# Kernel optimization log

Measured on AMD Instinct MI355X. Metric: run time of the kernel, lower is better.

Reference implementation:

```python
import jax, jax.numpy as jnp
import numpy as np

ALPHA = 0.2  # LeakyReLU negative slope
B, N, F, T, H, D = 4, 2048, 256, 8, 4, 64


def setup_inputs() -> dict:
    key = jax.random.key(0)
    ks = jax.random.split(key, 8)
    x = jax.random.normal(ks[0], (B, N, F), dtype=jnp.float32)
    adj = jax.random.randint(ks[1], (B, N, N), 0, 2, dtype=jnp.int32)
    type_idx = jax.random.randint(ks[2], (B, N), 0, T)
    type_onehot = jax.nn.one_hot(type_idx, T, dtype=jnp.float32)
    # per-head parameters stacked on a leading head axis (original uses H separate layers)
    s = 0.06  # ~xavier_uniform scale for these fan sizes
    Wq = jax.random.normal(ks[3], (H, F + T, D), dtype=jnp.float32) * s
    Wk = jax.random.normal(ks[4], (H, F + T, D), dtype=jnp.float32) * s
    W = jax.random.normal(ks[5], (H, F, D), dtype=jnp.float32) * s
    a = jax.random.normal(ks[6], (H, 2 * D, 1), dtype=jnp.float32) * s
    return {"x": x, "adj": adj, "type_onehot": type_onehot,
            "Wq": Wq, "Wk": Wk, "W": W, "a": a}


def reference(x, adj, type_onehot, Wq, Wk, W, a):
    # eval mode: dropout is identity
    nh, d = W.shape[0], W.shape[2]
    h_t = jnp.concatenate([x, type_onehot], axis=-1)           # (B,N,F+T)
    q = jnp.einsum('bnf,hfd->bhnd', h_t, Wq)                   # (B,H,N,D)
    k = jnp.einsum('bnf,hfd->bhnd', h_t, Wk)                   # (B,H,N,D)
    a1 = a[:, :d, 0]                                           # (H,D)
    a2 = a[:, d:, 0]                                           # (H,D)
    e1 = jnp.einsum('bhnd,hd->bhn', q, a1)                     # (B,H,N)
    e2 = jnp.einsum('bhnd,hd->bhn', k, a2)                     # (B,H,N)
    e = e1[:, :, :, None] + e2[:, :, None, :]                  # (B,H,N,N) additive score
    e = jnp.where(e > 0, e, ALPHA * e)                         # leaky relu
    mask = (adj > 0)[:, None, :, :]                            # (B,1,N,N)
    att = jnp.where(mask, e, jnp.float32(-9e15))
    att = jax.nn.softmax(att, axis=2)                          # torch dim=1 of (B,N,N) == axis 2 here
    att = att * adj[:, None, :, :].astype(att.dtype)
    Wh = jnp.einsum('bnf,hfd->bhnd', x, W)                     # (B,H,N,D)
    h_prime = jnp.einsum('bhij,bhjd->bhid', att, Wh)           # (B,H,N,D)
    out = jax.nn.elu(h_prime)                                  # concat=True per head
    # concat heads on feature dim, matching torch.cat([...], dim=2)
    return out.transpose(0, 2, 1, 3).reshape(x.shape[0], x.shape[1], nh * d)
```

## Files before the change

### kernel.cpp

```cpp
#include <hip/hip_runtime.h>
#include <hip/hip_bf16.h>
#include <math.h>

#define ALPHA 0.2f
#define LOG2E 1.4426950408889634f

constexpr int B_ = 4, N_ = 2048, F_ = 256, T_ = 8, H_ = 4, D_ = 64;
constexpr int FT = F_ + T_;

using half8   = __attribute__((ext_vector_type(8))) _Float16;
using float4v = __attribute__((ext_vector_type(4))) float;
using uint4v  = __attribute__((ext_vector_type(4))) unsigned;

#if __has_builtin(__builtin_amdgcn_exp2f)
#define EXP2F(x) __builtin_amdgcn_exp2f(x)
#else
#define EXP2F(x) exp2f(x)
#endif

__device__ inline unsigned pkrtz_u(float a, float b) {
    return __builtin_bit_cast(unsigned, __builtin_amdgcn_cvt_pkrtz(a, b));
}

#define V1_OFF    0u
#define V2_OFF    4224u
#define E1A_OFF   8448u
#define E2A_OFF   270592u
#define PARTS_OFF 794880u
#define WT_OFF    2892032u
#define BITS_OFF  3023104u
#define WHT_OFF   5120256u

__device__ inline void gl2lds16(const void* g, void* l) {
    __builtin_amdgcn_global_load_lds(
        (const __attribute__((address_space(1))) unsigned*)g,
        (__attribute__((address_space(3))) unsigned*)l, 16, 0, 0);
}

__global__ __launch_bounds__(256) void k_pre(const int* __restrict__ adj,
                                             const float* __restrict__ Wq,
                                             const float* __restrict__ Wk,
                                             const float* __restrict__ a,
                                             const float* __restrict__ W,
                                             unsigned* __restrict__ bits,
                                             float* __restrict__ v1,
                                             float* __restrict__ v2,
                                             _Float16* __restrict__ WT) {
    if (blockIdx.x < 65536u) {
        size_t tid = (size_t)blockIdx.x * 256 + threadIdx.x;
        int av = adj[tid];
        unsigned long long msk = __ballot(av != 0);
        int lane = threadIdx.x & 63;
        if (lane == 0)       bits[tid >> 5] = (unsigned)msk;
        else if (lane == 32) bits[tid >> 5] = (unsigned)(msk >> 32);
        return;
    }
    int gid = (blockIdx.x - 65536) * 256 + threadIdx.x;
    if (gid < 65536) {
        int hd = gid >> 8, f = gid & 255;
        int h = hd >> 6, d = hd & 63;
        WT[(size_t)hd * F_ + f] = (_Float16)W[((size_t)h * F_ + f) * D_ + d];
        return;
    }
    int tid = gid - 65536;
    if (tid >= 2 * H_ * FT) return;
    int sel = tid / (H_ * FT);
    int r = tid - sel * (H_ * FT);
    int h = r / FT, f = r - h * FT;
    const float* Wx = sel ? Wk : Wq;
    const float* av = a + h * 2 * D_ + sel * D_;
    const float* wrow = Wx + (size_t)(h * FT + f) * D_;
    float acc = 0.f;
    for (int d = 0; d < D_; ++d) acc += wrow[d] * av[d];
    (sel ? v2 : v1)[h * FT + f] = acc * LOG2E;
}

__global__ __launch_bounds__(256) void k_mid(const float* __restrict__ x,
                                             const float* __restrict__ oh,
                                             const float* __restrict__ v1,
                                             const float* __restrict__ v2,
                                             const _Float16* __restrict__ WT,
                                             float2* __restrict__ E1A,
                                             float2* __restrict__ E2A,
                                             _Float16* __restrict__ WhT) {
    if (blockIdx.x < 2048u) {
        int lane = threadIdx.x & 63;
        int w = threadIdx.x >> 6;
        int bn = blockIdx.x * 4 + w;
        int b = bn >> 11, n = bn & (N_ - 1);
        float a1h[H_] = {0.f, 0.f, 0.f, 0.f};
        float a2h[H_] = {0.f, 0.f, 0.f, 0.f};
        const float* xrow = x + (size_t)(b * N_ + n) * F_;
        for (int c = 0; c < 4; ++c) {
            int f = c * 64 + lane;
            float xv = xrow[f];
            #pragma unroll
            for (int h = 0; h < H_; ++h) {
                a1h[h] += xv * v1[h * FT + f];
                a2h[h] += xv * v2[h * FT + f];
            }
        }
        if (lane < T_) {
            float ov = oh[(size_t)(b * N_ + n) * T_ + lane];
            #pragma unroll
            for (int h = 0; h < H_; ++h) {
                a1h[h] += ov * v1[h * FT + F_ + lane];
                a2h[h] += ov * v2[h * FT + F_ + lane];
            }
        }
        #pragma unroll
        for (int off = 32; off; off >>= 1) {
            #pragma unroll
            for (int h = 0; h < H_; ++h) {
                a1h[h] += __shfl_xor(a1h[h], off, 64);
                a2h[h] += __shfl_xor(a2h[h], off, 64);
            }
        }
        if (lane == 0) {
            #pragma unroll
            for (int h = 0; h < H_; ++h) {
                size_t o = (size_t)(b * H_ + h) * N_ + n;
                E1A[o] = {EXP2F(a1h[h]), EXP2F(ALPHA * a1h[h])};
                E2A[o] = {EXP2F(a2h[h]), EXP2F(ALPHA * a2h[h])};
            }
        }
        return;
    }
    int bid = blockIdx.x - 2048;
    int jt = bid & 127, b = bid >> 7;
    int lane = threadIdx.x & 63;
    int h = threadIdx.x >> 6;
    int j0 = jt * 16;
    int m = lane & 15, quad = lane >> 4;
    float4v zero = {0.f, 0.f, 0.f, 0.f};
    float4v acc[4] = {zero, zero, zero, zero};
    #pragma unroll 2
    for (int f0 = 0; f0 < F_; f0 += 32) {
        const float* xp = x + (size_t)(b * N_ + j0 + m) * F_ + f0 + quad * 8;
        float4v xlo = *(const float4v*)xp;
        float4v xhi = *(const float4v*)(xp + 4);
        uint4v bp = {pkrtz_u(xlo[0], xlo[1]), pkrtz_u(xlo[2], xlo[3]),
                     pkrtz_u(xhi[0], xhi[1]), pkrtz_u(xhi[2], xhi[3])};
        half8 bfrag = __builtin_bit_cast(half8, bp);
        #pragma unroll
        for (int mt = 0; mt < 4; ++mt) {
            const _Float16* ap = WT + (size_t)(h * 64 + mt * 16 + m) * F_ + f0 + quad * 8;
            half8 afrag = *(const half8*)ap;
            acc[mt] = __builtin_amdgcn_mfma_f32_16x16x32_f16(afrag, bfrag, acc[mt], 0, 0, 0);
        }
    }
    #pragma unroll
    for (int mt = 0; mt < 4; ++mt) {
        #pragma unroll
        for (int reg = 0; reg < 4; ++reg) {
            int hd = h * 64 + mt * 16 + quad * 4 + reg;
            WhT[((size_t)b * 256 + hd) * N_ + j0 + m] = (_Float16)acc[mt][reg];
        }
    }
}

__global__ __launch_bounds__(256) void k_colsum(const unsigned* __restrict__ bits,
                                                const float2* __restrict__ E1A,
                                                const float2* __restrict__ E2A,
                                                float* __restrict__ part_s) {
    int tid = threadIdx.x;
    int jt = blockIdx.x, b = blockIdx.y, ic = blockIdx.z;
    int j = jt * 256 + tid;
    int i0 = ic * 128;
    float2 e2v[H_];
    float acc[H_] = {0.f, 0.f, 0.f, 0.f};
    #pragma unroll
    for (int h = 0; h < H_; ++h) e2v[h] = E2A[(size_t)(b * H_ + h) * N_ + j];
    const float2* e1b = E1A + (size_t)(b * H_) * N_;
    const unsigned* bp = bits + ((size_t)(b * N_ + i0)) * 64 + (j >> 5);
    unsigned sh = j & 31;
    #pragma unroll 8
    for (int k = 0; k < 128; ++k) {
        unsigned wv = bp[(size_t)k * 64];
        bool on = (wv >> sh) & 1u;
        int i = i0 + k;
        #pragma unroll
        for (int h = 0; h < H_; ++h) {
            float2 e1 = e1b[h * N_ + i];
            float t = fmaxf(e1.x * e2v[h].x, e1.y * e2v[h].y);
            acc[h] += on ? t : 0.f;
        }
    }
    #pragma unroll
    for (int h = 0; h < H_; ++h)
        part_s[(size_t)ic * (B_ * H_ * N_) + (size_t)(b * H_ + h) * N_ + j] = acc[h];
}

__global__ __launch_bounds__(256, 2) void k_main(const unsigned* __restrict__ bits,
                                                 const float2* __restrict__ E1A,
                                                 const float2* __restrict__ E2A,
                                                 const float* __restrict__ parts,
                                                 const _Float16* __restrict__ WhT,
                                                 float* __restrict__ out) {
    __shared__ float sPC[2048];
    __shared__ float sNC[2048];
    __shared__ unsigned sLUT[256][4];
    __shared__ _Float16 sW[2][8192];
    int lane = threadIdx.x;
    int wy = threadIdx.y;
    int it = blockIdx.x;
    int b  = blockIdx.y;
    int h  = blockIdx.z;
    int ibase = it * 64 + wy * 16;
    int m = lane & 15, quad = lane >> 4;
    int bh = b * H_ + h;
    int t256 = wy * 64 + lane;

    {
        unsigned t = t256;
        sLUT[t][0] = ((t & 1u) ? 0xFFFFu : 0u) | ((t & 2u) ? 0xFFFF0000u : 0u);
        sLUT[t][1] = ((t & 4u) ? 0xFFFFu : 0u) | ((t & 8u) ? 0xFFFF0000u : 0u);
        sLUT[t][2] = ((t & 16u) ? 0xFFFFu : 0u) | ((t & 32u) ? 0xFFFF0000u : 0u);
        sLUT[t][3] = ((t & 64u) ? 0xFFFFu : 0u) | ((t & 128u) ? 0xFFFF0000u : 0u);
        int base = t256 * 8;
        float4v s0 = {0.f, 0.f, 0.f, 0.f}, s1 = {0.f, 0.f, 0.f, 0.f};
        #pragma unroll
        for (int ic = 0; ic < 16; ++ic) {
            const float* pp = parts + (size_t)ic * (B_ * H_ * N_) + (size_t)bh * N_ + base;
            s0 += *(const float4v*)pp;
            s1 += *(const float4v*)(pp + 4);
        }
        const float2* e2p = E2A + (size_t)bh * N_ + base;
        #pragma unroll
        for (int e = 0; e < 4; ++e) {
            float s = s0[e];
            float c = (s > 0.f) ? 1.f / s : 0.f;
            float2 e2 = e2p[e];
            sPC[base + e] = e2.x * c;
            sNC[base + e] = e2.y * c;
        }
        #pragma unroll
        for (int e = 0; e < 4; ++e) {
            float s = s1[e];
            float c = (s > 0.f) ? 1.f / s : 0.f;
            float2 e2 = e2p[4 + e];
            sPC[base + 4 + e] = e2.x * c;
            sNC[base + 4 + e] = e2.y * c;
        }
    }
    float2 e1v = E1A[(size_t)bh * N_ + ibase + m];
    const _Float16* bbase = WhT + (size_t)(b * 256 + h * 64) * N_;
    const unsigned* brow = bits + ((size_t)(b * N_) + ibase + m) * 64;

    auto stage = [&](int buf, int jb) {
        #pragma unroll
        for (int q = 0; q < 4; ++q) {
            int r = q * 16 + wy * 4 + (lane >> 4);
            int g = (lane & 15) ^ (r & 15);
            const _Float16* gp = bbase + (size_t)r * N_ + jb + g * 8;
            void* lp = (void*)&sW[buf][q * 2048 + wy * 512];
            gl2lds16(gp, lp);
        }
    };

    stage(0, 0);
    __syncthreads();

    float4v zero = {0.f, 0.f, 0.f, 0.f};
    float4v acc[4] = {zero, zero, zero, zero};

    for (int k = 0; k < 16; ++k) {
        if (k < 15) stage((k + 1) & 1, (k + 1) * 128);
        uint4v bwv = *(const uint4v*)(brow + k * 4);
        #pragma unroll
        for (int u = 0; u < 4; ++u) {
            unsigned byte = (bwv[u] >> (quad * 8)) & 0xFFu;
            uint4v msk = *(const uint4v*)&sLUT[byte][0];
            int jg = k * 128 + u * 32 + quad * 8;
            float4v p0 = *(const float4v*)&sPC[jg];
            float4v p1 = *(const float4v*)&sPC[jg + 4];
            float4v n0 = *(const float4v*)&sNC[jg];
            float4v n1 = *(const float4v*)&sNC[jg + 4];
            float w[8];
            #pragma unroll
            for (int e = 0; e < 4; ++e) w[e]     = fmaxf(e1v.x * p0[e], e1v.y * n0[e]);
            #pragma unroll
            for (int e = 0; e < 4; ++e) w[4 + e] = fmaxf(e1v.x * p1[e], e1v.y * n1[e]);
            uint4v wvp = {pkrtz_u(w[0], w[1]) & msk[0], pkrtz_u(w[2], w[3]) & msk[1],
                          pkrtz_u(w[4], w[5]) & msk[2], pkrtz_u(w[6], w[7]) & msk[3]};
            half8 afrag = __builtin_bit_cast(half8, wvp);
            #pragma unroll
            for (int dt = 0; dt < 4; ++dt) {
                int r = dt * 16 + m;
                int segp = (u * 4 + quad) ^ m;
                half8 bfrag = *(const half8*)&sW[k & 1][r * 128 + segp * 8];
                acc[dt] = __builtin_amdgcn_mfma_f32_16x16x32_f16(afrag, bfrag, acc[dt], 0, 0, 0);
            }
        }
        __syncthreads();
    }

    #pragma unroll
    for (int dt = 0; dt < 4; ++dt) {
        #pragma unroll
        for (int reg = 0; reg < 4; ++reg) {
            int i = ibase + quad * 4 + reg;
            int d = dt * 16 + m;
            float v = acc[dt][reg];
            v = v > 0.f ? v : expm1f(v);
            out[((size_t)(b * N_ + i)) * (H_ * D_) + h * D_ + d] = v;
        }
    }
}

extern "C" void kernel_launch(void* const* d_in, const int* in_sizes, int n_in,
                              void* d_out, int out_size, void* d_ws, size_t ws_size,
                              hipStream_t stream) {
    const float* x   = (const float*)d_in[0];
    const int*   adj = (const int*)d_in[1];
    const float* oh  = (const float*)d_in[2];
    const float* Wq  = (const float*)d_in[3];
    const float* Wk  = (const float*)d_in[4];
    const float* W   = (const float*)d_in[5];
    const float* a   = (const float*)d_in[6];
    float* out = (float*)d_out;
    char* ws = (char*)d_ws;

    float*   v1    = (float*)(ws + V1_OFF);
    float*   v2    = (float*)(ws + V2_OFF);
    float2*  E1A   = (float2*)(ws + E1A_OFF);
    float2*  E2A   = (float2*)(ws + E2A_OFF);
    float*   parts = (float*)(ws + PARTS_OFF);
    _Float16* WT   = (_Float16*)(ws + WT_OFF);
    unsigned* bits = (unsigned*)(ws + BITS_OFF);
    _Float16* WhT  = (_Float16*)(ws + WHT_OFF);

    k_pre<<<65536 + 265, 256, 0, stream>>>(adj, Wq, Wk, a, W, bits, v1, v2, WT);
    k_mid<<<2048 + 512, 256, 0, stream>>>(x, oh, v1, v2, WT, E1A, E2A, WhT);
    k_colsum<<<dim3(8, 4, 16), 256, 0, stream>>>(bits, E1A, E2A, parts);
    k_main<<<dim3(32, 4, 4), dim3(64, 4), 0, stream>>>(bits, E1A, E2A, parts, WhT, out);
}
```

Baseline: 187.4 us.

## Vectorize adjacency bit-packing, cache E1 in LDS, double rows per wave in main

Adjacency packing now has each thread read four ints as a vector and combine nibbles with xor-shuffles, so the kernel needs a quarter as many blocks. The column-sum kernel stages E1 values in shared memory instead of rereading them from global memory every iteration. The main kernel gives each wave two 16-row tiles that share the staged WhT B-fragments and the sPC/sNC loads, which halves its grid. The LDS lookup table for masking is replaced by per-element selects. The cost is more registers per thread and fewer blocks in the main kernel, which may lower occupancy and parallelism.

```diff
diff --git a/kernel.cpp b/kernel.cpp
--- a/kernel.cpp
+++ b/kernel.cpp
@@ -10,6 +10,7 @@
 
 using half8   = __attribute__((ext_vector_type(8))) _Float16;
 using float4v = __attribute__((ext_vector_type(4))) float;
+using int4v   = __attribute__((ext_vector_type(4))) int;
 using uint4v  = __attribute__((ext_vector_type(4))) unsigned;
 
 #if __has_builtin(__builtin_amdgcn_exp2f)
@@ -46,16 +47,20 @@
                                              float* __restrict__ v1,
                                              float* __restrict__ v2,
                                              _Float16* __restrict__ WT) {
-    if (blockIdx.x < 65536u) {
-        size_t tid = (size_t)blockIdx.x * 256 + threadIdx.x;
-        int av = adj[tid];
-        unsigned long long msk = __ballot(av != 0);
+    if (blockIdx.x < 16384u) {
+        size_t t = (size_t)blockIdx.x * 256 + threadIdx.x;
         int lane = threadIdx.x & 63;
-        if (lane == 0)       bits[tid >> 5] = (unsigned)msk;
-        else if (lane == 32) bits[tid >> 5] = (unsigned)(msk >> 32);
+        int4v av = ((const int4v*)adj)[t];
+        unsigned nib = (av.x != 0 ? 1u : 0u) | (av.y != 0 ? 2u : 0u) |
+                       (av.z != 0 ? 4u : 0u) | (av.w != 0 ? 8u : 0u);
+        unsigned v = nib << ((lane & 7) * 4);
+        v |= __shfl_xor(v, 1, 64);
+        v |= __shfl_xor(v, 2, 64);
+        v |= __shfl_xor(v, 4, 64);
+        if ((lane & 7) == 0) bits[t >> 3] = v;
         return;
     }
-    int gid = (blockIdx.x - 65536) * 256 + threadIdx.x;
+    int gid = (blockIdx.x - 16384) * 256 + threadIdx.x;
     if (gid < 65536) {
         int hd = gid >> 8, f = gid & 255;
         int h = hd >> 6, d = hd & 63;
@@ -163,25 +168,31 @@
                                                 const float2* __restrict__ E1A,
                                                 const float2* __restrict__ E2A,
                                                 float* __restrict__ part_s) {
+    __shared__ float2 sE1[H_][128];
     int tid = threadIdx.x;
     int jt = blockIdx.x, b = blockIdx.y, ic = blockIdx.z;
     int j = jt * 256 + tid;
     int i0 = ic * 128;
+    #pragma unroll
+    for (int r = 0; r < 2; ++r) {
+        int idx = r * 256 + tid;
+        int hh = idx >> 7, ii = idx & 127;
+        sE1[hh][ii] = E1A[(size_t)(b * H_ + hh) * N_ + i0 + ii];
+    }
     float2 e2v[H_];
     float acc[H_] = {0.f, 0.f, 0.f, 0.f};
     #pragma unroll
     for (int h = 0; h < H_; ++h) e2v[h] = E2A[(size_t)(b * H_ + h) * N_ + j];
-    const float2* e1b = E1A + (size_t)(b * H_) * N_;
+    __syncthreads();
     const unsigned* bp = bits + ((size_t)(b * N_ + i0)) * 64 + (j >> 5);
     unsigned sh = j & 31;
     #pragma unroll 8
     for (int k = 0; k < 128; ++k) {
         unsigned wv = bp[(size_t)k * 64];
         bool on = (wv >> sh) & 1u;
-        int i = i0 + k;
         #pragma unroll
         for (int h = 0; h < H_; ++h) {
-            float2 e1 = e1b[h * N_ + i];
+            float2 e1 = sE1[h][k];
             float t = fmaxf(e1.x * e2v[h].x, e1.y * e2v[h].y);
             acc[h] += on ? t : 0.f;
         }
@@ -199,24 +210,18 @@
                                                  float* __restrict__ out) {
     __shared__ float sPC[2048];
     __shared__ float sNC[2048];
-    __shared__ unsigned sLUT[256][4];
     __shared__ _Float16 sW[2][8192];
     int lane = threadIdx.x;
     int wy = threadIdx.y;
     int it = blockIdx.x;
     int b  = blockIdx.y;
     int h  = blockIdx.z;
-    int ibase = it * 64 + wy * 16;
+    int ibase = it * 128 + wy * 32;
     int m = lane & 15, quad = lane >> 4;
     int bh = b * H_ + h;
     int t256 = wy * 64 + lane;
 
     {
-        unsigned t = t256;
-        sLUT[t][0] = ((t & 1u) ? 0xFFFFu : 0u) | ((t & 2u) ? 0xFFFF0000u : 0u);
-        sLUT[t][1] = ((t & 4u) ? 0xFFFFu : 0u) | ((t & 8u) ? 0xFFFF0000u : 0u);
-        sLUT[t][2] = ((t & 16u) ? 0xFFFFu : 0u) | ((t & 32u) ? 0xFFFF0000u : 0u);
-        sLUT[t][3] = ((t & 64u) ? 0xFFFFu : 0u) | ((t & 128u) ? 0xFFFF0000u : 0u);
         int base = t256 * 8;
         float4v s0 = {0.f, 0.f, 0.f, 0.f}, s1 = {0.f, 0.f, 0.f, 0.f};
         #pragma unroll
@@ -243,9 +248,11 @@
             sNC[base + 4 + e] = e2.y * c;
         }
     }
-    float2 e1v = E1A[(size_t)bh * N_ + ibase + m];
+    float2 e1vA = E1A[(size_t)bh * N_ + ibase + m];
+    float2 e1vB = E1A[(size_t)bh * N_ + ibase + 16 + m];
     const _Float16* bbase = WhT + (size_t)(b * 256 + h * 64) * N_;
-    const unsigned* brow = bits + ((size_t)(b * N_) + ibase + m) * 64;
+    const unsigned* browA = bits + ((size_t)(b * N_) + ibase + m) * 64;
+    const unsigned* browB = bits + ((size_t)(b * N_) + ibase + 16 + m) * 64;
 
     auto stage = [&](int buf, int jb) {
         #pragma unroll
@@ -262,34 +269,47 @@
     __syncthreads();
 
     float4v zero = {0.f, 0.f, 0.f, 0.f};
-    float4v acc[4] = {zero, zero, zero, zero};
+    float4v accA[4] = {zero, zero, zero, zero};
+    float4v accB[4] = {zero, zero, zero, zero};
 
     for (int k = 0; k < 16; ++k) {
         if (k < 15) stage((k + 1) & 1, (k + 1) * 128);
-        uint4v bwv = *(const uint4v*)(brow + k * 4);
+        uint4v bwA = *(const uint4v*)(browA + k * 4);
+        uint4v bwB = *(const uint4v*)(browB + k * 4);
         #pragma unroll
         for (int u = 0; u < 4; ++u) {
-            unsigned byte = (bwv[u] >> (quad * 8)) & 0xFFu;
-            uint4v msk = *(const uint4v*)&sLUT[byte][0];
+            unsigned wqA = bwA[u] >> (quad * 8);
+            unsigned wqB = bwB[u] >> (quad * 8);
             int jg = k * 128 + u * 32 + quad * 8;
             float4v p0 = *(const float4v*)&sPC[jg];
             float4v p1 = *(const float4v*)&sPC[jg + 4];
             float4v n0 = *(const float4v*)&sNC[jg];
             float4v n1 = *(const float4v*)&sNC[jg + 4];
-            float w[8];
-            #pragma unroll
-            for (int e = 0; e < 4; ++e) w[e]     = fmaxf(e1v.x * p0[e], e1v.y * n0[e]);
-            #pragma unroll
-            for (int e = 0; e < 4; ++e) w[4 + e] = fmaxf(e1v.x * p1[e], e1v.y * n1[e]);
-            uint4v wvp = {pkrtz_u(w[0], w[1]) & msk[0], pkrtz_u(w[2], w[3]) & msk[1],
-                          pkrtz_u(w[4], w[5]) & msk[2], pkrtz_u(w[6], w[7]) & msk[3]};
-            half8 afrag = __builtin_bit_cast(half8, wvp);
+            float wA[8], wB[8];
+            #pragma unroll
+            for (int e = 0; e < 4; ++e) {
+                float tA0 = fmaxf(e1vA.x * p0[e], e1vA.y * n0[e]);
+                float tA1 = fmaxf(e1vA.x * p1[e], e1vA.y * n1[e]);
+                wA[e]     = (wqA & (1u << e))  ? tA0 : 0.f;
+                wA[4 + e] = (wqA & (16u << e)) ? tA1 : 0.f;
+                float tB0 = fmaxf(e1vB.x * p0[e], e1vB.y * n0[e]);
+                float tB1 = fmaxf(e1vB.x * p1[e], e1vB.y * n1[e]);
+                wB[e]     = (wqB & (1u << e))  ? tB0 : 0.f;
+                wB[4 + e] = (wqB & (16u << e)) ? tB1 : 0.f;
+            }
+            uint4v wpA = {pkrtz_u(wA[0], wA[1]), pkrtz_u(wA[2], wA[3]),
+                          pkrtz_u(wA[4], wA[5]), pkrtz_u(wA[6], wA[7])};
+            uint4v wpB = {pkrtz_u(wB[0], wB[1]), pkrtz_u(wB[2], wB[3]),
+                          pkrtz_u(wB[4], wB[5]), pkrtz_u(wB[6], wB[7])};
+            half8 afA = __builtin_bit_cast(half8, wpA);
+            half8 afB = __builtin_bit_cast(half8, wpB);
             #pragma unroll
             for (int dt = 0; dt < 4; ++dt) {
                 int r = dt * 16 + m;
                 int segp = (u * 4 + quad) ^ m;
                 half8 bfrag = *(const half8*)&sW[k & 1][r * 128 + segp * 8];
-                acc[dt] = __builtin_amdgcn_mfma_f32_16x16x32_f16(afrag, bfrag, acc[dt], 0, 0, 0);
+                accA[dt] = __builtin_amdgcn_mfma_f32_16x16x32_f16(afA, bfrag, accA[dt], 0, 0, 0);
+                accB[dt] = __builtin_amdgcn_mfma_f32_16x16x32_f16(afB, bfrag, accB[dt], 0, 0, 0);
             }
         }
         __syncthreads();
@@ -299,11 +319,14 @@
     for (int dt = 0; dt < 4; ++dt) {
         #pragma unroll
         for (int reg = 0; reg < 4; ++reg) {
-            int i = ibase + quad * 4 + reg;
+            int iA = ibase + quad * 4 + reg;
             int d = dt * 16 + m;
-            float v = acc[dt][reg];
-            v = v > 0.f ? v : expm1f(v);
-            out[((size_t)(b * N_ + i)) * (H_ * D_) + h * D_ + d] = v;
+            float vA = accA[dt][reg];
+            vA = vA > 0.f ? vA : expm1f(vA);
+            out[((size_t)(b * N_ + iA)) * (H_ * D_) + h * D_ + d] = vA;
+            float vB = accB[dt][reg];
+            vB = vB > 0.f ? vB : expm1f(vB);
+            out[((size_t)(b * N_ + iA + 16)) * (H_ * D_) + h * D_ + d] = vB;
         }
     }
 }
@@ -330,8 +353,8 @@
     unsigned* bits = (unsigned*)(ws + BITS_OFF);
     _Float16* WhT  = (_Float16*)(ws + WHT_OFF);
 
-    k_pre<<<65536 + 265, 256, 0, stream>>>(adj, Wq, Wk, a, W, bits, v1, v2, WT);
+    k_pre<<<16384 + 265, 256, 0, stream>>>(adj, Wq, Wk, a, W, bits, v1, v2, WT);
     k_mid<<<2048 + 512, 256, 0, stream>>>(x, oh, v1, v2, WT, E1A, E2A, WhT);
     k_colsum<<<dim3(8, 4, 16), 256, 0, stream>>>(bits, E1A, E2A, parts);
-    k_main<<<dim3(32, 4, 4), dim3(64, 4), 0, stream>>>(bits, E1A, E2A, parts, WhT, out);
-}
+    k_main<<<dim3(16, 4, 4), dim3(64, 4), 0, stream>>>(bits, E1A, E2A, parts, WhT, out);
+}
```

New measurement: 180.4 us. 1.04x faster.

## Vectorize adjacency bit-packing, stage E1 in LDS, replace mask LUT with selects

Applied to the files above, without the earlier changes.

The adjacency packing kernel now has each thread load four ints as one vector and builds each 32-bit mask word with shuffle-xor reductions. This cuts the grid to a quarter of its size and widens the global loads on a bandwidth-bound pass. The column-sum kernel preloads its E1 slice into shared memory instead of rereading it from global for every row. The main kernel drops the 256-entry LDS mask lookup table and applies bits with per-element selects, trading LDS traffic for extra VALU work.

```diff
diff --git a/kernel.cpp b/kernel.cpp
--- a/kernel.cpp
+++ b/kernel.cpp
@@ -10,6 +10,7 @@
 
 using half8   = __attribute__((ext_vector_type(8))) _Float16;
 using float4v = __attribute__((ext_vector_type(4))) float;
+using int4v   = __attribute__((ext_vector_type(4))) int;
 using uint4v  = __attribute__((ext_vector_type(4))) unsigned;
 
 #if __has_builtin(__builtin_amdgcn_exp2f)
@@ -46,16 +47,20 @@
                                              float* __restrict__ v1,
                                              float* __restrict__ v2,
                                              _Float16* __restrict__ WT) {
-    if (blockIdx.x < 65536u) {
-        size_t tid = (size_t)blockIdx.x * 256 + threadIdx.x;
-        int av = adj[tid];
-        unsigned long long msk = __ballot(av != 0);
+    if (blockIdx.x < 16384u) {
+        size_t t = (size_t)blockIdx.x * 256 + threadIdx.x;
         int lane = threadIdx.x & 63;
-        if (lane == 0)       bits[tid >> 5] = (unsigned)msk;
-        else if (lane == 32) bits[tid >> 5] = (unsigned)(msk >> 32);
+        int4v av = ((const int4v*)adj)[t];
+        unsigned nib = (av.x != 0 ? 1u : 0u) | (av.y != 0 ? 2u : 0u) |
+                       (av.z != 0 ? 4u : 0u) | (av.w != 0 ? 8u : 0u);
+        unsigned v = nib << ((lane & 7) * 4);
+        v |= __shfl_xor(v, 1, 64);
+        v |= __shfl_xor(v, 2, 64);
+        v |= __shfl_xor(v, 4, 64);
+        if ((lane & 7) == 0) bits[t >> 3] = v;
         return;
     }
-    int gid = (blockIdx.x - 65536) * 256 + threadIdx.x;
+    int gid = (blockIdx.x - 16384) * 256 + threadIdx.x;
     if (gid < 65536) {
         int hd = gid >> 8, f = gid & 255;
         int h = hd >> 6, d = hd & 63;
@@ -163,25 +168,31 @@
                                                 const float2* __restrict__ E1A,
                                                 const float2* __restrict__ E2A,
                                                 float* __restrict__ part_s) {
+    __shared__ float2 sE1[H_][128];
     int tid = threadIdx.x;
     int jt = blockIdx.x, b = blockIdx.y, ic = blockIdx.z;
     int j = jt * 256 + tid;
     int i0 = ic * 128;
+    #pragma unroll
+    for (int r = 0; r < 2; ++r) {
+        int idx = r * 256 + tid;
+        int hh = idx >> 7, ii = idx & 127;
+        sE1[hh][ii] = E1A[(size_t)(b * H_ + hh) * N_ + i0 + ii];
+    }
     float2 e2v[H_];
     float acc[H_] = {0.f, 0.f, 0.f, 0.f};
     #pragma unroll
     for (int h = 0; h < H_; ++h) e2v[h] = E2A[(size_t)(b * H_ + h) * N_ + j];
-    const float2* e1b = E1A + (size_t)(b * H_) * N_;
+    __syncthreads();
     const unsigned* bp = bits + ((size_t)(b * N_ + i0)) * 64 + (j >> 5);
     unsigned sh = j & 31;
     #pragma unroll 8
     for (int k = 0; k < 128; ++k) {
         unsigned wv = bp[(size_t)k * 64];
         bool on = (wv >> sh) & 1u;
-        int i = i0 + k;
         #pragma unroll
         for (int h = 0; h < H_; ++h) {
-            float2 e1 = e1b[h * N_ + i];
+            float2 e1 = sE1[h][k];
             float t = fmaxf(e1.x * e2v[h].x, e1.y * e2v[h].y);
             acc[h] += on ? t : 0.f;
         }
@@ -199,7 +210,6 @@
                                                  float* __restrict__ out) {
     __shared__ float sPC[2048];
     __shared__ float sNC[2048];
-    __shared__ unsigned sLUT[256][4];
     __shared__ _Float16 sW[2][8192];
     int lane = threadIdx.x;
     int wy = threadIdx.y;
@@ -212,11 +222,6 @@
     int t256 = wy * 64 + lane;
 
     {
-        unsigned t = t256;
-        sLUT[t][0] = ((t & 1u) ? 0xFFFFu : 0u) | ((t & 2u) ? 0xFFFF0000u : 0u);
-        sLUT[t][1] = ((t & 4u) ? 0xFFFFu : 0u) | ((t & 8u) ? 0xFFFF0000u : 0u);
-        sLUT[t][2] = ((t & 16u) ? 0xFFFFu : 0u) | ((t & 32u) ? 0xFFFF0000u : 0u);
-        sLUT[t][3] = ((t & 64u) ? 0xFFFFu : 0u) | ((t & 128u) ? 0xFFFF0000u : 0u);
         int base = t256 * 8;
         float4v s0 = {0.f, 0.f, 0.f, 0.f}, s1 = {0.f, 0.f, 0.f, 0.f};
         #pragma unroll
@@ -269,8 +274,7 @@
         uint4v bwv = *(const uint4v*)(brow + k * 4);
         #pragma unroll
         for (int u = 0; u < 4; ++u) {
-            unsigned byte = (bwv[u] >> (quad * 8)) & 0xFFu;
-            uint4v msk = *(const uint4v*)&sLUT[byte][0];
+            unsigned wq = bwv[u] >> (quad * 8);
             int jg = k * 128 + u * 32 + quad * 8;
             float4v p0 = *(const float4v*)&sPC[jg];
             float4v p1 = *(const float4v*)&sPC[jg + 4];
@@ -278,11 +282,14 @@
             float4v n1 = *(const float4v*)&sNC[jg + 4];
             float w[8];
             #pragma unroll
-            for (int e = 0; e < 4; ++e) w[e]     = fmaxf(e1v.x * p0[e], e1v.y * n0[e]);
-            #pragma unroll
-            for (int e = 0; e < 4; ++e) w[4 + e] = fmaxf(e1v.x * p1[e], e1v.y * n1[e]);
-            uint4v wvp = {pkrtz_u(w[0], w[1]) & msk[0], pkrtz_u(w[2], w[3]) & msk[1],
-                          pkrtz_u(w[4], w[5]) & msk[2], pkrtz_u(w[6], w[7]) & msk[3]};
+            for (int e = 0; e < 4; ++e) {
+                float t0 = fmaxf(e1v.x * p0[e], e1v.y * n0[e]);
+                float t1 = fmaxf(e1v.x * p1[e], e1v.y * n1[e]);
+                w[e]     = (wq & (1u << e))  ? t0 : 0.f;
+                w[4 + e] = (wq & (16u << e)) ? t1 : 0.f;
+            }
+            uint4v wvp = {pkrtz_u(w[0], w[1]), pkrtz_u(w[2], w[3]),
+                          pkrtz_u(w[4], w[5]), pkrtz_u(w[6], w[7])};
             half8 afrag = __builtin_bit_cast(half8, wvp);
             #pragma unroll
             for (int dt = 0; dt < 4; ++dt) {
@@ -330,7 +337,7 @@
     unsigned* bits = (unsigned*)(ws + BITS_OFF);
     _Float16* WhT  = (_Float16*)(ws + WHT_OFF);
 
-    k_pre<<<65536 + 265, 256, 0, stream>>>(adj, Wq, Wk, a, W, bits, v1, v2, WT);
+    k_pre<<<16384 + 265, 256, 0, stream>>>(adj, Wq, Wk, a, W, bits, v1, v2, WT);
     k_mid<<<2048 + 512, 256, 0, stream>>>(x, oh, v1, v2, WT, E1A, E2A, WhT);
     k_colsum<<<dim3(8, 4, 16), 256, 0, stream>>>(bits, E1A, E2A, parts);
     k_main<<<dim3(32, 4, 4), dim3(64, 4), 0, stream>>>(bits, E1A, E2A, parts, WhT, out);
```

New measurement: 173.3 us (median of 2 runs). 1.08x faster.
